# Kernel tuning notes

Hardware: AMD Instinct MI355X
Metric: run time of the kernel (lower is better)

Reference implementation:

```python
import jax, jax.numpy as jnp
import numpy as np

N_NODES = 50000
N_EDGES = 1600000
IN_CH, HID_CH, OUT_CH = 128, 128, 64


def gcn_conv(x, src, dst, norm, W, b):
    # x: [N, d_in]; src/dst: [E'] (self-loops included); norm: [E']
    h = x @ W                                  # [N, d_out] transform first (dense GEMM)
    msg = h[src] * norm[:, None]               # [E', d_out] gather + scale
    out = jax.ops.segment_sum(msg, dst, num_segments=x.shape[0])  # scatter-add
    return out + b


def setup_inputs() -> dict:
    key = jax.random.key(0)
    k1, k2, k3, k4, k5, k6 = jax.random.split(key, 6)
    x = jax.random.normal(k1, (N_NODES, IN_CH), dtype=jnp.float32)
    edge_index = jax.random.randint(k2, (2, N_EDGES), 0, N_NODES, dtype=jnp.int64)
    # Glorot-style init for weights
    W1 = jax.random.normal(k3, (IN_CH, HID_CH), dtype=jnp.float32) / np.sqrt(IN_CH)
    b1 = jnp.zeros((HID_CH,), dtype=jnp.float32)
    W2 = jax.random.normal(k4, (HID_CH, OUT_CH), dtype=jnp.float32) / np.sqrt(HID_CH)
    b2 = jnp.zeros((OUT_CH,), dtype=jnp.float32)
    return {"x": x, "edge_index": edge_index, "W1": W1, "b1": b1, "W2": W2, "b2": b2}


def reference(x, edge_index, W1, b1, W2, b2):
    n = x.shape[0]
    # GCNConv default: add self-loops, symmetric normalization D^-1/2 (A+I) D^-1/2
    loop = jnp.arange(n, dtype=edge_index.dtype)
    src = jnp.concatenate([edge_index[0], loop])   # [E+N]
    dst = jnp.concatenate([edge_index[1], loop])   # [E+N]
    deg = jax.ops.segment_sum(jnp.ones_like(dst, dtype=x.dtype), dst, num_segments=n)
    dinv = jnp.where(deg > 0, jax.lax.rsqrt(deg), 0.0)  # [N]
    norm = dinv[src] * dinv[dst]                   # [E+N]

    h = gcn_conv(x, src, dst, norm, W1, b1)        # conv1
    h = jax.nn.relu(h)
    h = gcn_conv(h, src, dst, norm, W2, b2)        # conv2
    return jax.nn.log_softmax(h, axis=1)
```

## Files before the change

kernel.cpp:

```cpp
#include <hip/hip_runtime.h>
#include <hip/hip_bf16.h>
#include <math.h>


typedef unsigned int uint;
typedef unsigned short ushort_t;
typedef unsigned char uchar_t;
typedef __attribute__((ext_vector_type(8))) short bf16x8;
typedef __attribute__((ext_vector_type(4))) float f32x4;
typedef __attribute__((ext_vector_type(2))) float f32x2;

#define BSH 7
#define NBMAX 400
#define BIN_CHUNK 4096
#define CAP 6144

__device__ inline ushort_t f2b(float f) {
    uint u = __float_as_uint(f);
    return (ushort_t)((u + 0x7fffu + ((u >> 16) & 1u)) >> 16);
}

__device__ inline uchar_t f2e4m3_sw(float f) {
    float a = fabsf(f);
    a = fminf(a, 448.f);
    uint sign = (__float_as_uint(f) >> 24) & 0x80u;
    uint u = __float_as_uint(a);
    int e = (int)(u >> 23) - 127;
    uint code;
    if (e < -6) {
        float t = a * 512.0f;
        uint m = (uint)(t + 0.5f);
        code = (m > 7) ? 0x08u : m;
    } else {
        uint lsb = (u >> 20) & 1u;
        u += 0x0007FFFFu + lsb;
        e = (int)(u >> 23) - 127;
        if (e > 8) code = 0x7Eu;
        else code = ((uint)(e + 7) << 3) | ((u >> 20) & 7u);
    }
    return (uchar_t)(sign | code);
}
__device__ inline float e4m3_sw(uint c) {
    uint ef = (c >> 3) & 15u, m = c & 7u;
    float v = ef ? __uint_as_float(((ef + 120u) << 23) | (m << 20))
                 : (float)m * 0.001953125f;
    return (c & 0x80u) ? -v : v;
}

__device__ inline f32x2 fp8x2_lo(uint v) {
#if __has_builtin(__builtin_amdgcn_cvt_pk_f32_fp8)
    return __builtin_amdgcn_cvt_pk_f32_fp8(v, false);
#else
    return (f32x2){e4m3_sw(v & 255u), e4m3_sw((v >> 8) & 255u)};
#endif
}
__device__ inline f32x2 fp8x2_hi(uint v) {
#if __has_builtin(__builtin_amdgcn_cvt_pk_f32_fp8)
    return __builtin_amdgcn_cvt_pk_f32_fp8(v, true);
#else
    return (f32x2){e4m3_sw((v >> 16) & 255u), e4m3_sw((v >> 24) & 255u)};
#endif
}
__device__ inline uchar_t f32_fp8(float f) {
#if __has_builtin(__builtin_amdgcn_cvt_pk_fp8_f32)
    return (uchar_t)(__builtin_amdgcn_cvt_pk_fp8_f32(f, f, 0u, false) & 0xffu);
#else
    return f2e4m3_sw(f);
#endif
}

__global__ __launch_bounds__(256) void k_init(int* __restrict__ bktcnt, int nbk) {
    int i = blockIdx.x * 256 + threadIdx.x;
    if (i < nbk) bktcnt[i] = 0;
}

__global__ __launch_bounds__(256) void k_bin(const int* __restrict__ esrc, const int* __restrict__ edst,
                                             int* __restrict__ bktcnt, uint* __restrict__ bin,
                                             int e, int nbk) {
    __shared__ int hist[NBMAX];
    __shared__ int segbase[NBMAX];
    int tid = threadIdx.x;
    int b0 = blockIdx.x * BIN_CHUNK;
    int b1 = min(b0 + BIN_CHUNK, e);
    for (int i = tid; i < nbk; i += 256) hist[i] = 0;
    __syncthreads();
    for (int i = b0 + tid * 4; i < b1; i += 1024) {
        if (i + 4 <= b1) {
            int4 d = *(const int4*)&edst[i];
            atomicAdd(&hist[d.x >> BSH], 1);
            atomicAdd(&hist[d.y >> BSH], 1);
            atomicAdd(&hist[d.z >> BSH], 1);
            atomicAdd(&hist[d.w >> BSH], 1);
        } else {
            for (int j = i; j < b1; ++j) atomicAdd(&hist[edst[j] >> BSH], 1);
        }
    }
    __syncthreads();
    for (int b = tid; b < nbk; b += 256) {
        int c = hist[b];
        int gb = c ? atomicAdd(&bktcnt[b], c) : 0;
        segbase[b] = b * CAP + gb;
        hist[b] = 0;
    }
    __syncthreads();
    for (int i = b0 + tid * 4; i < b1; i += 1024) {
        if (i + 4 <= b1) {
            int4 d = *(const int4*)&edst[i];
            int4 s = *(const int4*)&esrc[i];
            int bx = d.x >> BSH, by = d.y >> BSH, bz = d.z >> BSH, bw = d.w >> BSH;
            int px = atomicAdd(&hist[bx], 1);
            int py = atomicAdd(&hist[by], 1);
            int pz = atomicAdd(&hist[bz], 1);
            int pw = atomicAdd(&hist[bw], 1);
            bin[segbase[bx] + px] = (uint)s.x | ((uint)(d.x & 127) << 17);
            bin[segbase[by] + py] = (uint)s.y | ((uint)(d.y & 127) << 17);
            bin[segbase[bz] + pz] = (uint)s.z | ((uint)(d.z & 127) << 17);
            bin[segbase[bw] + pw] = (uint)s.w | ((uint)(d.w & 127) << 17);
        } else {
            for (int j = i; j < b1; ++j) {
                int d = edst[j], s = esrc[j];
                int b = d >> BSH;
                int p = atomicAdd(&hist[b], 1);
                bin[segbase[b] + p] = (uint)s | ((uint)(d & 127) << 17);
            }
        }
    }
}

__global__ __launch_bounds__(512) void k_scanBkt(const int* __restrict__ bktcnt, int* __restrict__ bktoff,
                                                 int nbk) {
    int tid = threadIdx.x;
    int v = (tid < nbk) ? bktcnt[tid] : 0;
    int x = v;
    for (int off = 1; off < 64; off <<= 1) {
        int y = __shfl_up(x, off);
        if ((tid & 63) >= off) x += y;
    }
    __shared__ int wt[8];
    if ((tid & 63) == 63) wt[tid >> 6] = x;
    __syncthreads();
    int w = tid >> 6, woff = 0;
    for (int k = 0; k < w; ++k) woff += wt[k];
    if (tid < nbk) bktoff[tid] = x - v + woff;
}

__global__ __launch_bounds__(256) void k_bucket(const uint* __restrict__ bin, const int* __restrict__ bktcnt,
                                                const int* __restrict__ bktoff,
                                                int* __restrict__ rowstart, int* __restrict__ cnt,
                                                float* __restrict__ dinv, int* __restrict__ csr, int n) {
    __shared__ int lcnt[1 << BSH];
    __shared__ int cur[1 << BSH];
    __shared__ int wt[4];
    int b = blockIdx.x;
    int tid = threadIdx.x;
    int lo = b << BSH;
    int nl = min(1 << BSH, n - lo);
    int m = bktcnt[b];
    int base = b * CAP;
    int obase = bktoff[b];
    if (tid < (1 << BSH)) lcnt[tid] = 0;
    __syncthreads();
    for (int i = tid; i < m; i += 256) {
        uint v = bin[base + i];
        atomicAdd(&lcnt[v >> 17], 1);
    }
    __syncthreads();
    int v = (tid < (1 << BSH)) ? lcnt[tid] : 0;
    int x = v;
    for (int off = 1; off < 64; off <<= 1) {
        int y = __shfl_up(x, off);
        if ((tid & 63) >= off) x += y;
    }
    if ((tid & 63) == 63) wt[tid >> 6] = x;
    __syncthreads();
    int excl = x - v + ((tid >= 64 && tid < 128) ? wt[0] : 0);
    if (tid < nl) {
        int node = lo + tid;
        rowstart[node] = obase + excl;
        cnt[node] = v;
        dinv[node] = rsqrtf((float)(v + 1));
        cur[tid] = obase + excl;
    }
    __syncthreads();
    for (int i = tid; i < m; i += 256) {
        uint en = bin[base + i];
        int dl = en >> 17;
        int p = atomicAdd(&cur[dl], 1);
        csr[p] = (int)(en & 0x1FFFFu);
    }
}

__global__ __launch_bounds__(256) void k_cvtW(const float* __restrict__ W1, const float* __restrict__ W2,
                                              ushort_t* __restrict__ W1t, ushort_t* __restrict__ W2t) {
    int i = blockIdx.x * 256 + threadIdx.x;
    if (i < 16384) {
        int k = i >> 7, nn = i & 127;
        W1t[nn * 128 + k] = f2b(W1[k * 128 + nn]);
    } else if (i < 16384 + 8192) {
        int j = i - 16384;
        int k = j >> 6, nn = j & 63;
        W2t[nn * 128 + k] = f2b(W2[k * 64 + nn]);
    }
}

template <int COLS, bool XBF16, bool OUTFP8>
__global__ __launch_bounds__(256) void k_mgemm(const void* __restrict__ Xv, const ushort_t* __restrict__ Wt,
                                               const float* __restrict__ dinv,
                                               void* __restrict__ Yv, int nrows) {
    constexpr int NT = COLS / 16;
    __shared__ ushort_t lsX[64 * 128];
    __shared__ ushort_t lsW[COLS * 128];
    int tid = threadIdx.x;
    int rbase = blockIdx.x * 64;

#pragma unroll
    for (int it = 0; it < 4; ++it) {
        int idx = (tid + it * 256) * 8;
        int r = idx >> 7, c = idx & 127;
        int grow = rbase + r;
        uint4 pv = make_uint4(0, 0, 0, 0);
        if (grow < nrows) {
            if (XBF16) {
                pv = *(const uint4*)((const ushort_t*)Xv + (size_t)grow * 128 + c);
            } else {
                const float* xp = (const float*)Xv + (size_t)grow * 128 + c;
                float4 a = *(const float4*)xp;
                float4 b = *(const float4*)(xp + 4);
                pv.x = (uint)f2b(a.x) | ((uint)f2b(a.y) << 16);
                pv.y = (uint)f2b(a.z) | ((uint)f2b(a.w) << 16);
                pv.z = (uint)f2b(b.x) | ((uint)f2b(b.y) << 16);
                pv.w = (uint)f2b(b.z) | ((uint)f2b(b.w) << 16);
            }
        }
        int boff = (r * 256 + c * 2) ^ ((r & 7) << 4);
        *(uint4*)((char*)lsX + boff) = pv;
    }
#pragma unroll
    for (int it = 0; it < NT; ++it) {
        int idx = (tid + it * 256) * 8;
        int nr = idx >> 7, k = idx & 127;
        uint4 v = *(const uint4*)&Wt[nr * 128 + k];
        int boff = (nr * 256 + k * 2) ^ ((nr & 7) << 4);
        *(uint4*)((char*)lsW + boff) = v;
    }
    __syncthreads();

    int w = tid >> 6, l = tid & 63;
    int lr = l & 15, lg = l >> 4;
    int xrow = w * 16 + lr;
    bf16x8 a[4];
#pragma unroll
    for (int ks = 0; ks < 4; ++ks) {
        int boff = (xrow * 256 + (ks * 32 + lg * 8) * 2) ^ ((xrow & 7) << 4);
        a[ks] = *(const bf16x8*)((const char*)lsX + boff);
    }
    f32x4 acc[NT];
#pragma unroll
    for (int ct = 0; ct < NT; ++ct) {
        acc[ct] = (f32x4){0.f, 0.f, 0.f, 0.f};
#pragma unroll
        for (int ks = 0; ks < 4; ++ks) {
            int wrow = ct * 16 + lr;
            int boff = (wrow * 256 + (ks * 32 + lg * 8) * 2) ^ ((wrow & 7) << 4);
            bf16x8 b = *(const bf16x8*)((const char*)lsW + boff);
            acc[ct] = __builtin_amdgcn_mfma_f32_16x16x32_bf16(a[ks], b, acc[ct], 0, 0, 0);
        }
    }
    float dr[4];
#pragma unroll
    for (int r = 0; r < 4; ++r) {
        int row = rbase + w * 16 + lg * 4 + r;
        dr[r] = (OUTFP8 && row < nrows) ? dinv[row] : 1.f;
    }
#pragma unroll
    for (int ct = 0; ct < NT; ++ct) {
        int ch = ct * 16 + lr;
#pragma unroll
        for (int r = 0; r < 4; ++r) {
            int row = rbase + w * 16 + lg * 4 + r;
            if (row < nrows) {
                if (OUTFP8) ((uchar_t*)Yv)[(size_t)row * COLS + ch] = f32_fp8(dr[r] * acc[ct][r]);
                else        ((ushort_t*)Yv)[(size_t)row * COLS + ch] = f2b(acc[ct][r]);
            }
        }
    }
}

__global__ __launch_bounds__(256) void k_agg1(const uchar_t* __restrict__ t1,
                                              const int* __restrict__ csr,
                                              const int* __restrict__ rowstart, const int* __restrict__ cnt,
                                              const float* __restrict__ dinv, const float* __restrict__ b1,
                                              uint* __restrict__ h, int n) {
    int tid = threadIdx.x;
    int i = blockIdx.x * 4 + (tid >> 6);
    if (i >= n) return;
    int lane = tid & 63;
    int half = lane >> 5, cl = lane & 31;
    float a0 = 0.f, a1 = 0.f, a2 = 0.f, a3 = 0.f;
    if (half == 0) {
        uint v = *(const uint*)(t1 + ((size_t)i << 7) + cl * 4);
        f32x2 lo = fp8x2_lo(v), hi = fp8x2_hi(v);
        a0 = lo.x; a1 = lo.y; a2 = hi.x; a3 = hi.y;
    }
    int beg = rowstart[i], m = cnt[i];
    int j = 0;
    for (; j + 8 <= m; j += 8) {
        int c = csr[beg + j + (lane & 7)];
        int s0 = __shfl(c, 0 + half);
        int s1 = __shfl(c, 2 + half);
        int s2 = __shfl(c, 4 + half);
        int s3 = __shfl(c, 6 + half);
        uint v0 = *(const uint*)(t1 + ((size_t)s0 << 7) + cl * 4);
        uint v1 = *(const uint*)(t1 + ((size_t)s1 << 7) + cl * 4);
        uint v2 = *(const uint*)(t1 + ((size_t)s2 << 7) + cl * 4);
        uint v3 = *(const uint*)(t1 + ((size_t)s3 << 7) + cl * 4);
        f32x2 p;
        p = fp8x2_lo(v0); a0 += p.x; a1 += p.y;  p = fp8x2_hi(v0); a2 += p.x; a3 += p.y;
        p = fp8x2_lo(v1); a0 += p.x; a1 += p.y;  p = fp8x2_hi(v1); a2 += p.x; a3 += p.y;
        p = fp8x2_lo(v2); a0 += p.x; a1 += p.y;  p = fp8x2_hi(v2); a2 += p.x; a3 += p.y;
        p = fp8x2_lo(v3); a0 += p.x; a1 += p.y;  p = fp8x2_hi(v3); a2 += p.x; a3 += p.y;
    }
    for (; j < m; j += 2) {
        int idx = j + half;
        if (idx < m) {
            int s = csr[beg + idx];
            uint v = *(const uint*)(t1 + ((size_t)s << 7) + cl * 4);
            f32x2 p;
            p = fp8x2_lo(v); a0 += p.x; a1 += p.y;
            p = fp8x2_hi(v); a2 += p.x; a3 += p.y;
        }
    }
    a0 += __shfl_xor(a0, 32); a1 += __shfl_xor(a1, 32);
    a2 += __shfl_xor(a2, 32); a3 += __shfl_xor(a3, 32);
    float di = dinv[i];
    float4 bb = ((const float4*)b1)[cl];
    float o0 = fmaxf(fmaf(di, a0, bb.x), 0.f);
    float o1 = fmaxf(fmaf(di, a1, bb.y), 0.f);
    float o2 = fmaxf(fmaf(di, a2, bb.z), 0.f);
    float o3 = fmaxf(fmaf(di, a3, bb.w), 0.f);
    if (half == 0) {
        uint2 pk;
        pk.x = (uint)f2b(o0) | ((uint)f2b(o1) << 16);
        pk.y = (uint)f2b(o2) | ((uint)f2b(o3) << 16);
        *(uint2*)&h[((size_t)i << 6) + cl * 2] = pk;
    }
}

__global__ __launch_bounds__(256) void k_agg2(const uchar_t* __restrict__ t2,
                                              const int* __restrict__ csr,
                                              const int* __restrict__ rowstart, const int* __restrict__ cnt,
                                              const float* __restrict__ dinv, const float* __restrict__ b2,
                                              float* __restrict__ out, int n) {
    int tid = threadIdx.x;
    int i = blockIdx.x * 4 + (tid >> 6);
    if (i >= n) return;
    int lane = tid & 63;
    int q = lane >> 4, cl = lane & 15;
    float a0 = 0.f, a1 = 0.f, a2 = 0.f, a3 = 0.f;
    if (q == 0) {
        uint v = *(const uint*)(t2 + ((size_t)i << 6) + cl * 4);
        f32x2 lo = fp8x2_lo(v), hi = fp8x2_hi(v);
        a0 = lo.x; a1 = lo.y; a2 = hi.x; a3 = hi.y;
    }
    int beg = rowstart[i], m = cnt[i];
    int j = 0;
    for (; j + 8 <= m; j += 8) {
        int c = csr[beg + j + (lane & 7)];
        int s0 = __shfl(c, 0 + q);
        int s1 = __shfl(c, 4 + q);
        uint v0 = *(const uint*)(t2 + ((size_t)s0 << 6) + cl * 4);
        uint v1 = *(const uint*)(t2 + ((size_t)s1 << 6) + cl * 4);
        f32x2 p;
        p = fp8x2_lo(v0); a0 += p.x; a1 += p.y;  p = fp8x2_hi(v0); a2 += p.x; a3 += p.y;
        p = fp8x2_lo(v1); a0 += p.x; a1 += p.y;  p = fp8x2_hi(v1); a2 += p.x; a3 += p.y;
    }
    for (; j < m; j += 4) {
        int idx = j + q;
        if (idx < m) {
            int s = csr[beg + idx];
            uint v = *(const uint*)(t2 + ((size_t)s << 6) + cl * 4);
            f32x2 p;
            p = fp8x2_lo(v); a0 += p.x; a1 += p.y;
            p = fp8x2_hi(v); a2 += p.x; a3 += p.y;
        }
    }
    a0 += __shfl_xor(a0, 16); a1 += __shfl_xor(a1, 16);
    a2 += __shfl_xor(a2, 16); a3 += __shfl_xor(a3, 16);
    a0 += __shfl_xor(a0, 32); a1 += __shfl_xor(a1, 32);
    a2 += __shfl_xor(a2, 32); a3 += __shfl_xor(a3, 32);
    float di = dinv[i];
    float4 bb = ((const float4*)b2)[cl];
    float o0 = fmaf(di, a0, bb.x);
    float o1 = fmaf(di, a1, bb.y);
    float o2 = fmaf(di, a2, bb.z);
    float o3 = fmaf(di, a3, bb.w);
    float mx = fmaxf(fmaxf(o0, o1), fmaxf(o2, o3));
    mx = fmaxf(mx, __shfl_xor(mx, 1));
    mx = fmaxf(mx, __shfl_xor(mx, 2));
    mx = fmaxf(mx, __shfl_xor(mx, 4));
    mx = fmaxf(mx, __shfl_xor(mx, 8));
    float s = expf(o0 - mx) + expf(o1 - mx) + expf(o2 - mx) + expf(o3 - mx);
    s += __shfl_xor(s, 1);
    s += __shfl_xor(s, 2);
    s += __shfl_xor(s, 4);
    s += __shfl_xor(s, 8);
    float ls = mx + logf(s);
    if (lane < 16) {
        float4 r = make_float4(o0 - ls, o1 - ls, o2 - ls, o3 - ls);
        *(float4*)&out[((size_t)i << 6) + cl * 4] = r;
    }
}

extern "C" void kernel_launch(void* const* d_in, const int* in_sizes, int n_in,
                              void* d_out, int out_size, void* d_ws, size_t ws_size,
                              hipStream_t stream) {
    const float* x  = (const float*)d_in[0];
    const int* eidx = (const int*)d_in[1];
    const float* W1 = (const float*)d_in[2];
    const float* b1 = (const float*)d_in[3];
    const float* W2 = (const float*)d_in[4];
    const float* b2 = (const float*)d_in[5];
    float* out = (float*)d_out;

    const int n = in_sizes[0] / 128;
    const int e = in_sizes[1] / 2;
    const int* esrc = eidx;
    const int* edst = eidx + e;
    const int nbk = (n + (1 << BSH) - 1) >> BSH;

    size_t off = 0;
    auto carve = [&](size_t bytes) {
        void* p = (char*)d_ws + off;
        off += (bytes + 255) & ~(size_t)255;
        return p;
    };
    uchar_t*  xW1  = (uchar_t*)carve((size_t)n * 128);
    ushort_t* h    = (ushort_t*)carve((size_t)n * 128 * 2);
    uchar_t*  hW2  = (uchar_t*)carve((size_t)n * 64);
    ushort_t* W1t  = (ushort_t*)carve(128 * 128 * 2);
    ushort_t* W2t  = (ushort_t*)carve(64 * 128 * 2);
    int*   cnt     = (int*)carve((size_t)n * 4);
    float* dinv    = (float*)carve((size_t)n * 4);
    int*   rowstart= (int*)carve((size_t)n * 4);
    int*   bktcnt  = (int*)carve((size_t)nbk * 4);
    int*   bktoff  = (int*)carve((size_t)nbk * 4);
    uint*  bin     = (uint*)carve((size_t)nbk * CAP * 4);
    int*   csr     = (int*)carve((size_t)e * 4);
    (void)ws_size;

    const int nbBin  = (e + BIN_CHUNK - 1) / BIN_CHUNK;
    const int nbWave = (n + 3) / 4;
    const int nbGemm = (n + 63) / 64;

    k_init<<<(nbk + 255) / 256, 256, 0, stream>>>(bktcnt, nbk);
    k_bin<<<nbBin, 256, 0, stream>>>(esrc, edst, bktcnt, bin, e, nbk);
    k_scanBkt<<<1, 512, 0, stream>>>(bktcnt, bktoff, nbk);
    k_bucket<<<nbk, 256, 0, stream>>>(bin, bktcnt, bktoff, rowstart, cnt, dinv, csr, n);
    k_cvtW<<<96, 256, 0, stream>>>(W1, W2, W1t, W2t);

    k_mgemm<128, false, true><<<nbGemm, 256, 0, stream>>>(x, W1t, dinv, xW1, n);
    k_agg1<<<nbWave, 256, 0, stream>>>(xW1, csr, rowstart, cnt, dinv, b1, (uint*)h, n);

    k_mgemm<64, true, true><<<nbGemm, 256, 0, stream>>>(h, W2t, dinv, hW2, n);
    k_agg2<<<nbWave, 256, 0, stream>>>(hW2, csr, rowstart, cnt, dinv, b2, out, n);
}
```

Measured before the change: 148.5 us.

## Split layer-1 aggregation into two 64-channel halves with prefetched CSR indices

The first GEMM now writes its fp8 output as two separate 64-column planes, and the layer-1 aggregation runs as two launches, one per half. Each half's gather table is N×64 bytes (~3.2MB) instead of N×128, which should fit better in cache for the random gathers. Both aggregation kernels also prefetch the next group of CSR indices one iteration ahead. In exchange the CSR index list is read twice and there is an extra launch.

Measured after the change: 162.7 us. 1.1x slower.

```diff
diff --git a/kernel.cpp b/kernel.cpp
--- a/kernel.cpp
+++ b/kernel.cpp
@@ -203,7 +203,7 @@
     }
 }
 
-template <int COLS, bool XBF16, bool OUTFP8>
+template <int COLS, bool XBF16, bool OUTFP8, bool OUTSPLIT>
 __global__ __launch_bounds__(256) void k_mgemm(const void* __restrict__ Xv, const ushort_t* __restrict__ Wt,
                                                const float* __restrict__ dinv,
                                                void* __restrict__ Yv, int nrows) {
@@ -279,70 +279,75 @@
         for (int r = 0; r < 4; ++r) {
             int row = rbase + w * 16 + lg * 4 + r;
             if (row < nrows) {
-                if (OUTFP8) ((uchar_t*)Yv)[(size_t)row * COLS + ch] = f32_fp8(dr[r] * acc[ct][r]);
-                else        ((ushort_t*)Yv)[(size_t)row * COLS + ch] = f2b(acc[ct][r]);
+                if (OUTFP8) {
+                    size_t addr = OUTSPLIT
+                        ? (size_t)(ch >> 6) * ((size_t)nrows * 64) + (size_t)row * 64 + (ch & 63)
+                        : (size_t)row * COLS + ch;
+                    ((uchar_t*)Yv)[addr] = f32_fp8(dr[r] * acc[ct][r]);
+                } else {
+                    ((ushort_t*)Yv)[(size_t)row * COLS + ch] = f2b(acc[ct][r]);
+                }
             }
         }
     }
 }
 
-__global__ __launch_bounds__(256) void k_agg1(const uchar_t* __restrict__ t1,
-                                              const int* __restrict__ csr,
-                                              const int* __restrict__ rowstart, const int* __restrict__ cnt,
-                                              const float* __restrict__ dinv, const float* __restrict__ b1,
-                                              uint* __restrict__ h, int n) {
+__global__ __launch_bounds__(256) void k_agg1h(const uchar_t* __restrict__ t1,
+                                               const int* __restrict__ csr,
+                                               const int* __restrict__ rowstart, const int* __restrict__ cnt,
+                                               const float* __restrict__ dinv, const float* __restrict__ b1,
+                                               uint* __restrict__ h, int n, int q) {
     int tid = threadIdx.x;
     int i = blockIdx.x * 4 + (tid >> 6);
     if (i >= n) return;
     int lane = tid & 63;
-    int half = lane >> 5, cl = lane & 31;
+    int g = lane >> 4, cl = lane & 15;
     float a0 = 0.f, a1 = 0.f, a2 = 0.f, a3 = 0.f;
-    if (half == 0) {
-        uint v = *(const uint*)(t1 + ((size_t)i << 7) + cl * 4);
+    if (g == 0) {
+        uint v = *(const uint*)(t1 + ((size_t)i << 6) + cl * 4);
         f32x2 lo = fp8x2_lo(v), hi = fp8x2_hi(v);
         a0 = lo.x; a1 = lo.y; a2 = hi.x; a3 = hi.y;
     }
     int beg = rowstart[i], m = cnt[i];
     int j = 0;
-    for (; j + 8 <= m; j += 8) {
-        int c = csr[beg + j + (lane & 7)];
-        int s0 = __shfl(c, 0 + half);
-        int s1 = __shfl(c, 2 + half);
-        int s2 = __shfl(c, 4 + half);
-        int s3 = __shfl(c, 6 + half);
-        uint v0 = *(const uint*)(t1 + ((size_t)s0 << 7) + cl * 4);
-        uint v1 = *(const uint*)(t1 + ((size_t)s1 << 7) + cl * 4);
-        uint v2 = *(const uint*)(t1 + ((size_t)s2 << 7) + cl * 4);
-        uint v3 = *(const uint*)(t1 + ((size_t)s3 << 7) + cl * 4);
+    int c = (m >= 8) ? csr[beg + (lane & 7)] : 0;
+    for (; j + 8 <= m; ) {
+        int jn = j + 8;
+        int cn = (jn + 8 <= m) ? csr[beg + jn + (lane & 7)] : 0;
+        int s0 = __shfl(c, 0 + g);
+        int s1 = __shfl(c, 4 + g);
+        uint v0 = *(const uint*)(t1 + ((size_t)s0 << 6) + cl * 4);
+        uint v1 = *(const uint*)(t1 + ((size_t)s1 << 6) + cl * 4);
         f32x2 p;
         p = fp8x2_lo(v0); a0 += p.x; a1 += p.y;  p = fp8x2_hi(v0); a2 += p.x; a3 += p.y;
         p = fp8x2_lo(v1); a0 += p.x; a1 += p.y;  p = fp8x2_hi(v1); a2 += p.x; a3 += p.y;
-        p = fp8x2_lo(v2); a0 += p.x; a1 += p.y;  p = fp8x2_hi(v2); a2 += p.x; a3 += p.y;
-        p = fp8x2_lo(v3); a0 += p.x; a1 += p.y;  p = fp8x2_hi(v3); a2 += p.x; a3 += p.y;
-    }
-    for (; j < m; j += 2) {
-        int idx = j + half;
+        c = cn; j = jn;
+    }
+    for (; j < m; j += 4) {
+        int idx = j + g;
         if (idx < m) {
             int s = csr[beg + idx];
-            uint v = *(const uint*)(t1 + ((size_t)s << 7) + cl * 4);
+            uint v = *(const uint*)(t1 + ((size_t)s << 6) + cl * 4);
             f32x2 p;
             p = fp8x2_lo(v); a0 += p.x; a1 += p.y;
             p = fp8x2_hi(v); a2 += p.x; a3 += p.y;
         }
     }
+    a0 += __shfl_xor(a0, 16); a1 += __shfl_xor(a1, 16);
+    a2 += __shfl_xor(a2, 16); a3 += __shfl_xor(a3, 16);
     a0 += __shfl_xor(a0, 32); a1 += __shfl_xor(a1, 32);
     a2 += __shfl_xor(a2, 32); a3 += __shfl_xor(a3, 32);
-    float di = dinv[i];
-    float4 bb = ((const float4*)b1)[cl];
-    float o0 = fmaxf(fmaf(di, a0, bb.x), 0.f);
-    float o1 = fmaxf(fmaf(di, a1, bb.y), 0.f);
-    float o2 = fmaxf(fmaf(di, a2, bb.z), 0.f);
-    float o3 = fmaxf(fmaf(di, a3, bb.w), 0.f);
-    if (half == 0) {
+    if (lane < 16) {
+        float di = dinv[i];
+        float4 bb = ((const float4*)b1)[q * 16 + cl];
+        float o0 = fmaxf(fmaf(di, a0, bb.x), 0.f);
+        float o1 = fmaxf(fmaf(di, a1, bb.y), 0.f);
+        float o2 = fmaxf(fmaf(di, a2, bb.z), 0.f);
+        float o3 = fmaxf(fmaf(di, a3, bb.w), 0.f);
         uint2 pk;
         pk.x = (uint)f2b(o0) | ((uint)f2b(o1) << 16);
         pk.y = (uint)f2b(o2) | ((uint)f2b(o3) << 16);
-        *(uint2*)&h[((size_t)i << 6) + cl * 2] = pk;
+        *(uint2*)&h[((size_t)i << 6) + q * 32 + cl * 2] = pk;
     }
 }
 
@@ -355,27 +360,30 @@
     int i = blockIdx.x * 4 + (tid >> 6);
     if (i >= n) return;
     int lane = tid & 63;
-    int q = lane >> 4, cl = lane & 15;
+    int g = lane >> 4, cl = lane & 15;
     float a0 = 0.f, a1 = 0.f, a2 = 0.f, a3 = 0.f;
-    if (q == 0) {
+    if (g == 0) {
         uint v = *(const uint*)(t2 + ((size_t)i << 6) + cl * 4);
         f32x2 lo = fp8x2_lo(v), hi = fp8x2_hi(v);
         a0 = lo.x; a1 = lo.y; a2 = hi.x; a3 = hi.y;
     }
     int beg = rowstart[i], m = cnt[i];
     int j = 0;
-    for (; j + 8 <= m; j += 8) {
-        int c = csr[beg + j + (lane & 7)];
-        int s0 = __shfl(c, 0 + q);
-        int s1 = __shfl(c, 4 + q);
+    int c = (m >= 8) ? csr[beg + (lane & 7)] : 0;
+    for (; j + 8 <= m; ) {
+        int jn = j + 8;
+        int cn = (jn + 8 <= m) ? csr[beg + jn + (lane & 7)] : 0;
+        int s0 = __shfl(c, 0 + g);
+        int s1 = __shfl(c, 4 + g);
         uint v0 = *(const uint*)(t2 + ((size_t)s0 << 6) + cl * 4);
         uint v1 = *(const uint*)(t2 + ((size_t)s1 << 6) + cl * 4);
         f32x2 p;
         p = fp8x2_lo(v0); a0 += p.x; a1 += p.y;  p = fp8x2_hi(v0); a2 += p.x; a3 += p.y;
         p = fp8x2_lo(v1); a0 += p.x; a1 += p.y;  p = fp8x2_hi(v1); a2 += p.x; a3 += p.y;
+        c = cn; j = jn;
     }
     for (; j < m; j += 4) {
-        int idx = j + q;
+        int idx = j + g;
         if (idx < m) {
             int s = csr[beg + idx];
             uint v = *(const uint*)(t2 + ((size_t)s << 6) + cl * 4);
@@ -458,9 +466,11 @@
     k_bucket<<<nbk, 256, 0, stream>>>(bin, bktcnt, bktoff, rowstart, cnt, dinv, csr, n);
     k_cvtW<<<96, 256, 0, stream>>>(W1, W2, W1t, W2t);
 
-    k_mgemm<128, false, true><<<nbGemm, 256, 0, stream>>>(x, W1t, dinv, xW1, n);
-    k_agg1<<<nbWave, 256, 0, stream>>>(xW1, csr, rowstart, cnt, dinv, b1, (uint*)h, n);
-
-    k_mgemm<64, true, true><<<nbGemm, 256, 0, stream>>>(h, W2t, dinv, hW2, n);
+    k_mgemm<128, false, true, true><<<nbGemm, 256, 0, stream>>>(x, W1t, dinv, xW1, n);
+    for (int q = 0; q < 2; ++q)
+        k_agg1h<<<nbWave, 256, 0, stream>>>(xW1 + (size_t)q * n * 64, csr, rowstart, cnt,
+                                            dinv, b1, (uint*)h, n, q);
+
+    k_mgemm<64, true, true, false><<<nbGemm, 256, 0, stream>>>(h, W2t, dinv, hW2, n);
     k_agg2<<<nbWave, 256, 0, stream>>>(hW2, csr, rowstart, cnt, dinv, b2, out, n);
 }
```
